# Optimization experiments

Hardware: AMD Instinct MI355X
Metric: run time of the kernel (lower is better)

Reference implementation:

```python
import jax, jax.numpy as jnp
import numpy as np

B, H, W, C = 4, 180, 320, 64
ATTN_SCALE = 0.125  # C ** -0.5
EPS = 1e-6  # flax LayerNorm default epsilon


def _layer_norm(x, scale, bias):
    mu = jnp.mean(x, axis=-1, keepdims=True)
    var = jnp.mean(jnp.square(x - mu), axis=-1, keepdims=True)
    return (x - mu) * jax.lax.rsqrt(var + EPS) * scale + bias


def setup_inputs() -> dict:
    key = jax.random.key(0)
    ks = jax.random.split(key, 8)
    w_init = 1.0 / np.sqrt(C)  # lecun_normal-ish scale for CxC dense kernels
    return {
        "x_l": jax.random.normal(ks[0], (B, H, W, C), jnp.float32),
        "x_r": jax.random.normal(ks[1], (B, H, W, C), jnp.float32),
        "ln_l_scale": jnp.ones((C,), jnp.float32),
        "ln_l_bias": jnp.zeros((C,), jnp.float32),
        "ln_r_scale": jnp.ones((C,), jnp.float32),
        "ln_r_bias": jnp.zeros((C,), jnp.float32),
        "w_ql": jax.random.normal(ks[2], (C, C), jnp.float32) * w_init,
        "b_ql": jnp.zeros((C,), jnp.float32),
        "w_qr": jax.random.normal(ks[3], (C, C), jnp.float32) * w_init,
        "b_qr": jnp.zeros((C,), jnp.float32),
        "w_vl": jax.random.normal(ks[4], (C, C), jnp.float32) * w_init,
        "b_vl": jnp.zeros((C,), jnp.float32),
        "w_vr": jax.random.normal(ks[5], (C, C), jnp.float32) * w_init,
        "b_vr": jnp.zeros((C,), jnp.float32),
        "beta": jax.random.normal(ks[6], (1, 1, 1, C), jnp.float32) * 0.1,
        "gamma": jax.random.normal(ks[7], (1, 1, 1, C), jnp.float32) * 0.1,
    }


def reference(x_l, x_r, ln_l_scale, ln_l_bias, ln_r_scale, ln_r_bias,
              w_ql, b_ql, w_qr, b_qr, w_vl, b_vl, w_vr, b_vr, beta, gamma):
    # Projections (attention runs along the width axis, per (b, h) scanline)
    q_l = _layer_norm(x_l, ln_l_scale, ln_l_bias) @ w_ql + b_ql   # [B,H,W,C]
    q_r = _layer_norm(x_r, ln_r_scale, ln_r_bias) @ w_qr + b_qr   # [B,H,W,C]
    v_l = x_l @ w_vl + b_vl                                       # [B,H,W,C]
    v_r = x_r @ w_vr + b_vr                                       # [B,H,W,C]

    # Shared score matrix: [B, H, W_l, W_r]
    attn = jnp.einsum('bhlc,bhrc->bhlr', q_l, q_r) * ATTN_SCALE

    # Row softmax (over W_r) attends right->left
    f_r2l = jnp.einsum('bhlr,bhrc->bhlc', jax.nn.softmax(attn, axis=-1), v_r) * beta
    # Column softmax (over W_l) attends left->right
    f_l2r = jnp.einsum('bhlr,bhlc->bhrc', jax.nn.softmax(attn, axis=-2), v_l) * gamma

    return (x_l + f_r2l, x_r + f_l2r)
```

## Files before the change

### kernel.cpp

```cpp
#include <hip/hip_runtime.h>
#include <hip/hip_bf16.h>

#define NB 4
#define NH 180
#define NW 320
#define NC 64
#define NSCAN (NB*NH)
#define NROWS (NB*NH*NW)
#define NELEM ((size_t)NROWS*NC)

using short8  = __attribute__((ext_vector_type(8))) short;
using floatx4 = __attribute__((ext_vector_type(4))) float;

__device__ __forceinline__ float bflo(unsigned int u) { return __uint_as_float(u << 16); }
__device__ __forceinline__ float bfhi(unsigned int u) { return __uint_as_float(u & 0xffff0000u); }

__device__ __forceinline__ unsigned short fbf(float f) {
    __hip_bfloat16 h = __float2bfloat16(f);
    unsigned short s; __builtin_memcpy(&s, &h, 2); return s;
}
__device__ __forceinline__ unsigned int packbf(float lo, float hi) {
    return (unsigned int)fbf(lo) | ((unsigned int)fbf(hi) << 16);
}

#define SCALE_LOG2E 0.18033688011112042f

__global__ __launch_bounds__(256) void proj_kernel(
    const float* __restrict__ xl, const float* __restrict__ xr,
    const float* __restrict__ lsl, const float* __restrict__ lbl,
    const float* __restrict__ lsr, const float* __restrict__ lbr,
    const float* __restrict__ wql, const float* __restrict__ bql,
    const float* __restrict__ wqr, const float* __restrict__ bqr,
    const float* __restrict__ wvl, const float* __restrict__ bvl,
    const float* __restrict__ wvr, const float* __restrict__ bvr,
    __hip_bfloat16* __restrict__ ql, __hip_bfloat16* __restrict__ qr,
    __hip_bfloat16* __restrict__ vlT, __hip_bfloat16* __restrict__ vrT)
{
    const int p    = blockIdx.y;
    const int t    = threadIdx.x;
    const int row0 = blockIdx.x * 256;

    const float* src  = (p == 0 || p == 2) ? xl : xr;
    const float* Wm   = (p == 0) ? wql : (p == 1) ? wqr : (p == 2) ? wvl : wvr;
    const float* bias = (p == 0) ? bql : (p == 1) ? bqr : (p == 2) ? bvl : bvr;
    __hip_bfloat16* dst = (p == 0) ? ql : (p == 1) ? qr : (p == 2) ? vlT : vrT;
    const bool doLN = (p < 2);
    const float* lns = (p == 0) ? lsl : lsr;
    const float* lnb = (p == 0) ? lbl : lbr;
    const float oscale = (p == 0) ? SCALE_LOG2E : 1.0f;

    __shared__ __align__(16) __hip_bfloat16 sA[256 * 72];
    __shared__ __align__(16) __hip_bfloat16 sWt[64 * 72];
    __shared__ float sLs[64], sLb[64], sBias[64];

    if (t < 64) {
        sLs[t]   = doLN ? lns[t] : 1.0f;
        sLb[t]   = doLN ? lnb[t] : 0.0f;
        sBias[t] = bias[t];
    }
    {
        const int k  = t >> 2;
        const int c0 = (t & 3) * 16;
        const float4* wrow = (const float4*)(Wm + k * NC + c0);
        float wv[16];
#pragma unroll
        for (int j = 0; j < 4; ++j) {
            float4 w4 = wrow[j];
            wv[4*j] = w4.x; wv[4*j+1] = w4.y; wv[4*j+2] = w4.z; wv[4*j+3] = w4.w;
        }
#pragma unroll
        for (int j = 0; j < 16; ++j)
            sWt[(c0 + j) * 72 + k] = __float2bfloat16(wv[j]);
    }
    __syncthreads();

    {
        const float4* x4 = (const float4*)(src + (size_t)(row0 + t) * NC);
        float f[64];
#pragma unroll
        for (int j = 0; j < 16; ++j) {
            float4 v = x4[j];
            f[4*j] = v.x; f[4*j+1] = v.y; f[4*j+2] = v.z; f[4*j+3] = v.w;
        }
        if (doLN) {
            float s = 0.f, s2 = 0.f;
#pragma unroll
            for (int c = 0; c < 64; ++c) { s += f[c]; s2 = fmaf(f[c], f[c], s2); }
            const float mu   = s * (1.0f / 64.0f);
            const float var  = s2 * (1.0f / 64.0f) - mu * mu;
            const float rstd = rsqrtf(var + 1e-6f);
#pragma unroll
            for (int c = 0; c < 64; ++c) f[c] = (f[c] - mu) * rstd * sLs[c] + sLb[c];
        }
        unsigned int* arow = (unsigned int*)&sA[t * 72];
#pragma unroll
        for (int j = 0; j < 32; ++j) arow[j] = packbf(f[2*j], f[2*j+1]);
    }
    __syncthreads();

    const int lane = t & 63;
    const int wv_  = t >> 6;
    const int quad = lane >> 4;
    const int mn   = lane & 15;

    short8 bfr[4][2];
#pragma unroll
    for (int nt = 0; nt < 4; ++nt)
#pragma unroll
        for (int ks = 0; ks < 2; ++ks)
            bfr[nt][ks] = *(const short8*)&sWt[(nt * 16 + mn) * 72 + ks * 32 + quad * 8];

#pragma unroll
    for (int mt = 0; mt < 4; ++mt) {
        const int rl = wv_ * 64 + mt * 16 + mn;
        short8 a0 = *(const short8*)&sA[rl * 72 +      quad * 8];
        short8 a1 = *(const short8*)&sA[rl * 72 + 32 + quad * 8];
#pragma unroll
        for (int nt = 0; nt < 4; ++nt) {
            floatx4 c = {0.f, 0.f, 0.f, 0.f};
            c = __builtin_amdgcn_mfma_f32_16x16x32_bf16(a0, bfr[nt][0], c, 0, 0, 0);
            c = __builtin_amdgcn_mfma_f32_16x16x32_bf16(a1, bfr[nt][1], c, 0, 0, 0);
            const int col = nt * 16 + mn;
            const float bb = sBias[col];
            if (p < 2) {
#pragma unroll
                for (int i = 0; i < 4; ++i) {
                    const int rowl = wv_ * 64 + mt * 16 + quad * 4 + i;
                    dst[(size_t)(row0 + rowl) * NC + col] =
                        __float2bfloat16((c[i] + bb) * oscale);
                }
            } else {
#pragma unroll
                for (int i = 0; i < 4; ++i) {
                    const unsigned grow = (unsigned)(row0 + wv_ * 64 + mt * 16 + quad * 4 + i);
                    const unsigned sc   = grow / 320u;
                    const unsigned wr   = grow - sc * 320u;
                    dst[(size_t)sc * (NC * NW) + (unsigned)col * NW + wr] =
                        __float2bfloat16(c[i] + bb);
                }
            }
        }
    }
}

__global__ __launch_bounds__(256) void attn_kernel(
    const __hip_bfloat16* __restrict__ ql, const __hip_bfloat16* __restrict__ qr,
    const __hip_bfloat16* __restrict__ vlT, const __hip_bfloat16* __restrict__ vrT,
    const float* __restrict__ xl, const float* __restrict__ xr,
    const float* __restrict__ beta, const float* __restrict__ gamma,
    float* __restrict__ out)
{
    const int flat = blockIdx.x + 5 * (blockIdx.y + 720 * blockIdx.z);
    const int g    = (flat & 7) * 900 + (flat >> 3);
    const int mt   = g % 5;
    const int s2   = g / 5;
    const int p    = s2 & 1;
    const int scan = s2 >> 1;

    const int t    = threadIdx.x;
    const int lane = t & 63;
    const int w    = t >> 6;
    const int quad = lane >> 4;
    const int mn   = lane & 15;
    const int m0   = mt * 64;

    const __hip_bfloat16* Q  = (p ? qr  : ql ) + (size_t)scan * (NW * NC);
    const __hip_bfloat16* K  = (p ? ql  : qr ) + (size_t)scan * (NW * NC);
    const __hip_bfloat16* VT = (p ? vlT : vrT) + (size_t)scan * (NC * NW);
    const float* xS = p ? xr : xl;
    const float* gv = p ? gamma : beta;

    __shared__ __align__(16) __hip_bfloat16 sQP[64 * 72];
    __shared__ __align__(16) char sU[18432];
    __shared__ float sRS[64];
    __hip_bfloat16* sK  = (__hip_bfloat16*)sU;
    __hip_bfloat16* sVt = (__hip_bfloat16*)(sU + 9216);
    float* sO = (float*)sU;

    const int sr  = t >> 2;
    const int sc0 = (t & 3) * 16;

    uint4 rk0, rk1, rv0, rv1;
    {
        const uint4* gk = (const uint4*)(K + (size_t)sr * NC + sc0);
        rk0 = gk[0]; rk1 = gk[1];
        const uint4* gt = (const uint4*)(VT + (size_t)sr * NW + sc0);
        rv0 = gt[0]; rv1 = gt[1];
    }

    {
        const uint4* gq = (const uint4*)(Q + (size_t)(m0 + sr) * NC + sc0);
        uint4 a = gq[0], b = gq[1];
        uint4* d = (uint4*)&sQP[sr * 72 + sc0];
        d[0] = a; d[1] = b;
    }
    __syncthreads();

    const short8 qa0 = *(const short8*)&sQP[(w * 16 + mn) * 72 +      quad * 8];
    const short8 qa1 = *(const short8*)&sQP[(w * 16 + mn) * 72 + 32 + quad * 8];

    floatx4 acc[4];
#pragma unroll
    for (int nt = 0; nt < 4; ++nt) acc[nt] = (floatx4){0.f, 0.f, 0.f, 0.f};
    float rs = 0.f;

    for (int rb = 0; rb < NW; rb += 64) {
        __syncthreads();
        {
            uint4* dk = (uint4*)&sK [sr * 72 + sc0]; dk[0] = rk0; dk[1] = rk1;
            uint4* dv = (uint4*)&sVt[sr * 72 + sc0]; dv[0] = rv0; dv[1] = rv1;
        }
        __syncthreads();

        if (rb + 64 < NW) {
            const uint4* gk = (const uint4*)(K + (size_t)(rb + 64 + sr) * NC + sc0);
            rk0 = gk[0]; rk1 = gk[1];
            const uint4* gt = (const uint4*)(VT + (size_t)sr * NW + (rb + 64) + sc0);
            rv0 = gt[0]; rv1 = gt[1];
        }

        __builtin_amdgcn_s_setprio(1);
#pragma unroll
        for (int rt = 0; rt < 4; ++rt) {
            short8 ka0 = *(const short8*)&sK[(rt * 16 + mn) * 72 +      quad * 8];
            short8 ka1 = *(const short8*)&sK[(rt * 16 + mn) * 72 + 32 + quad * 8];
            floatx4 s = {0.f, 0.f, 0.f, 0.f};
            s = __builtin_amdgcn_mfma_f32_16x16x32_bf16(ka0, qa0, s, 0, 0, 0);
            s = __builtin_amdgcn_mfma_f32_16x16x32_bf16(ka1, qa1, s, 0, 0, 0);
            const unsigned c0 = packbf(exp2f(s[0]), exp2f(s[1]));
            const unsigned c1 = packbf(exp2f(s[2]), exp2f(s[3]));
            rs += bflo(c0) + bfhi(c0) + bflo(c1) + bfhi(c1);
            uint2 pk; pk.x = c0; pk.y = c1;
            *(uint2*)&sQP[(w * 16 + mn) * 72 + rt * 16 + quad * 4] = pk;
        }

#pragma unroll
        for (int ks = 0; ks < 2; ++ks) {
            short8 pa = *(const short8*)&sQP[(w * 16 + mn) * 72 + ks * 32 + quad * 8];
#pragma unroll
            for (int nt = 0; nt < 4; ++nt) {
                short8 vb = *(const short8*)&sVt[(nt * 16 + mn) * 72 + ks * 32 + quad * 8];
                acc[nt] = __builtin_amdgcn_mfma_f32_16x16x32_bf16(pa, vb, acc[nt], 0, 0, 0);
            }
        }
        __builtin_amdgcn_s_setprio(0);
    }

    rs += __shfl_xor(rs, 16);
    rs += __shfl_xor(rs, 32);

    __syncthreads();

    if (lane < 16) sRS[w * 16 + lane] = 1.0f / rs;
#pragma unroll
    for (int nt = 0; nt < 4; ++nt)
#pragma unroll
        for (int i = 0; i < 4; ++i)
            sO[(w * 16 + quad * 4 + i) * 68 + nt * 16 + mn] = acc[nt][i];
    __syncthreads();

    {
        const int m = t >> 2, c0 = (t & 3) * 16;
        const float inv = sRS[m];
        const int grow = scan * NW + m0 + m;
        const float4* xg = (const float4*)(xS + (size_t)grow * NC + c0);
        const float4* gg = (const float4*)(gv + c0);
        const float4* so = (const float4*)&sO[m * 68 + c0];
        float4* og = (float4*)(out + (p ? NELEM : (size_t)0) + (size_t)grow * NC + c0);
#pragma unroll
        for (int j = 0; j < 4; ++j) {
            float4 xv = xg[j];
            float4 gvv = gg[j];
            float4 ov = so[j];
            float4 o;
            o.x = xv.x + ov.x * inv * gvv.x;
            o.y = xv.y + ov.y * inv * gvv.y;
            o.z = xv.z + ov.z * inv * gvv.z;
            o.w = xv.w + ov.w * inv * gvv.w;
            og[j] = o;
        }
    }
}

extern "C" void kernel_launch(void* const* d_in, const int* in_sizes, int n_in,
                              void* d_out, int out_size, void* d_ws, size_t ws_size,
                              hipStream_t stream)
{
    const float* xl  = (const float*)d_in[0];
    const float* xr  = (const float*)d_in[1];
    const float* lsl = (const float*)d_in[2];
    const float* lbl = (const float*)d_in[3];
    const float* lsr = (const float*)d_in[4];
    const float* lbr = (const float*)d_in[5];
    const float* wql = (const float*)d_in[6];
    const float* bql = (const float*)d_in[7];
    const float* wqr = (const float*)d_in[8];
    const float* bqr = (const float*)d_in[9];
    const float* wvl = (const float*)d_in[10];
    const float* bvl = (const float*)d_in[11];
    const float* wvr = (const float*)d_in[12];
    const float* bvr = (const float*)d_in[13];
    const float* beta  = (const float*)d_in[14];
    const float* gamma = (const float*)d_in[15];

    __hip_bfloat16* ws   = (__hip_bfloat16*)d_ws;
    __hip_bfloat16* ql_  = ws;
    __hip_bfloat16* qr_  = ws + NELEM;
    __hip_bfloat16* vlT_ = ws + 2 * NELEM;
    __hip_bfloat16* vrT_ = ws + 3 * NELEM;

    proj_kernel<<<dim3(NROWS / 256, 4, 1), 256, 0, stream>>>(
        xl, xr, lsl, lbl, lsr, lbr, wql, bql, wqr, bqr, wvl, bvl, wvr, bvr,
        ql_, qr_, vlT_, vrT_);

    attn_kernel<<<dim3(5, NSCAN, 2), 256, 0, stream>>>(
        ql_, qr_, vlT_, vrT_, xl, xr, beta, gamma, (float*)d_out);
}
```

Before: 375.0 us.

## Read K/V fragments directly from global, per-wave LDS buffers, swizzle proj grid

The attention kernel no longer stages K and V^T tiles through shared memory with block-wide barriers. Each wave now loads its MFMA operand fragments straight from global memory (relying on L1/L2 caching) and keeps a private LDS buffer for the P tile and output staging, which removes every __syncthreads. The softmax row sum is now accumulated in fp32 before bf16 rounding. Launch bounds are raised to 5 blocks per SM to favor occupancy. The projection kernel's block order is also remapped with an XCD-style interleave. The trade-off is that each wave issues redundant global loads instead of sharing one staged copy, which adds cache traffic.

```diff
diff --git a/kernel.cpp b/kernel.cpp
--- a/kernel.cpp
+++ b/kernel.cpp
@@ -36,9 +36,15 @@
     __hip_bfloat16* __restrict__ ql, __hip_bfloat16* __restrict__ qr,
     __hip_bfloat16* __restrict__ vlT, __hip_bfloat16* __restrict__ vrT)
 {
-    const int p    = blockIdx.y;
+    const int flat = blockIdx.x + 900 * blockIdx.y;
+    const int g    = (flat & 7) * 450 + (flat >> 3);
+    const int kind = g & 1;
+    const int pairid = g >> 1;
+    const int side = pairid & 1;
+    const int tile = pairid >> 1;
+    const int p    = side + 2 * kind;
     const int t    = threadIdx.x;
-    const int row0 = blockIdx.x * 256;
+    const int row0 = tile * 256;
 
     const float* src  = (p == 0 || p == 2) ? xl : xr;
     const float* Wm   = (p == 0) ? wql : (p == 1) ? wqr : (p == 2) ? wvl : wvr;
@@ -143,7 +149,7 @@
     }
 }
 
-__global__ __launch_bounds__(256) void attn_kernel(
+__global__ __launch_bounds__(256, 5) void attn_kernel(
     const __hip_bfloat16* __restrict__ ql, const __hip_bfloat16* __restrict__ qr,
     const __hip_bfloat16* __restrict__ vlT, const __hip_bfloat16* __restrict__ vrT,
     const float* __restrict__ xl, const float* __restrict__ xr,
@@ -170,34 +176,14 @@
     const float* xS = p ? xr : xl;
     const float* gv = p ? gamma : beta;
 
-    __shared__ __align__(16) __hip_bfloat16 sQP[64 * 72];
-    __shared__ __align__(16) char sU[18432];
+    __shared__ __align__(16) char sW[4 * 4608];
     __shared__ float sRS[64];
-    __hip_bfloat16* sK  = (__hip_bfloat16*)sU;
-    __hip_bfloat16* sVt = (__hip_bfloat16*)(sU + 9216);
-    float* sO = (float*)sU;
-
-    const int sr  = t >> 2;
-    const int sc0 = (t & 3) * 16;
-
-    uint4 rk0, rk1, rv0, rv1;
-    {
-        const uint4* gk = (const uint4*)(K + (size_t)sr * NC + sc0);
-        rk0 = gk[0]; rk1 = gk[1];
-        const uint4* gt = (const uint4*)(VT + (size_t)sr * NW + sc0);
-        rv0 = gt[0]; rv1 = gt[1];
-    }
-
-    {
-        const uint4* gq = (const uint4*)(Q + (size_t)(m0 + sr) * NC + sc0);
-        uint4 a = gq[0], b = gq[1];
-        uint4* d = (uint4*)&sQP[sr * 72 + sc0];
-        d[0] = a; d[1] = b;
-    }
-    __syncthreads();
-
-    const short8 qa0 = *(const short8*)&sQP[(w * 16 + mn) * 72 +      quad * 8];
-    const short8 qa1 = *(const short8*)&sQP[(w * 16 + mn) * 72 + 32 + quad * 8];
+    __hip_bfloat16* sP  = (__hip_bfloat16*)(sW + w * 4608);
+    float*          sOw = (float*)(sW + w * 4608);
+
+    const __hip_bfloat16* qrow = Q + (size_t)(m0 + w * 16 + mn) * NC;
+    const short8 qa0 = *(const short8*)(qrow + quad * 8);
+    const short8 qa1 = *(const short8*)(qrow + 32 + quad * 8);
 
     floatx4 acc[4];
 #pragma unroll
@@ -205,41 +191,30 @@
     float rs = 0.f;
 
     for (int rb = 0; rb < NW; rb += 64) {
-        __syncthreads();
-        {
-            uint4* dk = (uint4*)&sK [sr * 72 + sc0]; dk[0] = rk0; dk[1] = rk1;
-            uint4* dv = (uint4*)&sVt[sr * 72 + sc0]; dv[0] = rv0; dv[1] = rv1;
-        }
-        __syncthreads();
-
-        if (rb + 64 < NW) {
-            const uint4* gk = (const uint4*)(K + (size_t)(rb + 64 + sr) * NC + sc0);
-            rk0 = gk[0]; rk1 = gk[1];
-            const uint4* gt = (const uint4*)(VT + (size_t)sr * NW + (rb + 64) + sc0);
-            rv0 = gt[0]; rv1 = gt[1];
-        }
-
         __builtin_amdgcn_s_setprio(1);
 #pragma unroll
         for (int rt = 0; rt < 4; ++rt) {
-            short8 ka0 = *(const short8*)&sK[(rt * 16 + mn) * 72 +      quad * 8];
-            short8 ka1 = *(const short8*)&sK[(rt * 16 + mn) * 72 + 32 + quad * 8];
+            const __hip_bfloat16* kr = K + (size_t)(rb + rt * 16 + mn) * NC + quad * 8;
+            const short8 ka0 = *(const short8*)kr;
+            const short8 ka1 = *(const short8*)(kr + 32);
             floatx4 s = {0.f, 0.f, 0.f, 0.f};
             s = __builtin_amdgcn_mfma_f32_16x16x32_bf16(ka0, qa0, s, 0, 0, 0);
             s = __builtin_amdgcn_mfma_f32_16x16x32_bf16(ka1, qa1, s, 0, 0, 0);
-            const unsigned c0 = packbf(exp2f(s[0]), exp2f(s[1]));
-            const unsigned c1 = packbf(exp2f(s[2]), exp2f(s[3]));
-            rs += bflo(c0) + bfhi(c0) + bflo(c1) + bfhi(c1);
-            uint2 pk; pk.x = c0; pk.y = c1;
-            *(uint2*)&sQP[(w * 16 + mn) * 72 + rt * 16 + quad * 4] = pk;
+            const float e0 = exp2f(s[0]), e1 = exp2f(s[1]);
+            const float e2 = exp2f(s[2]), e3 = exp2f(s[3]);
+            rs += (e0 + e1) + (e2 + e3);
+            uint2 pk; pk.x = packbf(e0, e1); pk.y = packbf(e2, e3);
+            *(uint2*)&sP[mn * 72 + rt * 16 + quad * 4] = pk;
         }
 
 #pragma unroll
         for (int ks = 0; ks < 2; ++ks) {
-            short8 pa = *(const short8*)&sQP[(w * 16 + mn) * 72 + ks * 32 + quad * 8];
+            const short8 pa = *(const short8*)&sP[mn * 72 + ks * 32 + quad * 8];
 #pragma unroll
             for (int nt = 0; nt < 4; ++nt) {
-                short8 vb = *(const short8*)&sVt[(nt * 16 + mn) * 72 + ks * 32 + quad * 8];
+                const __hip_bfloat16* vr =
+                    VT + (size_t)(nt * 16 + mn) * NW + rb + ks * 32 + quad * 8;
+                const short8 vb = *(const short8*)vr;
                 acc[nt] = __builtin_amdgcn_mfma_f32_16x16x32_bf16(pa, vb, acc[nt], 0, 0, 0);
             }
         }
@@ -249,15 +224,13 @@
     rs += __shfl_xor(rs, 16);
     rs += __shfl_xor(rs, 32);
 
-    __syncthreads();
-
     if (lane < 16) sRS[w * 16 + lane] = 1.0f / rs;
+
 #pragma unroll
     for (int nt = 0; nt < 4; ++nt)
 #pragma unroll
         for (int i = 0; i < 4; ++i)
-            sO[(w * 16 + quad * 4 + i) * 68 + nt * 16 + mn] = acc[nt][i];
-    __syncthreads();
+            sOw[(quad * 4 + i) * 68 + nt * 16 + mn] = acc[nt][i];
 
     {
         const int m = t >> 2, c0 = (t & 3) * 16;
@@ -265,7 +238,8 @@
         const int grow = scan * NW + m0 + m;
         const float4* xg = (const float4*)(xS + (size_t)grow * NC + c0);
         const float4* gg = (const float4*)(gv + c0);
-        const float4* so = (const float4*)&sO[m * 68 + c0];
+        const float4* so = (const float4*)((const float*)(sW + (m >> 4) * 4608)
+                                           + (m & 15) * 68 + c0);
         float4* og = (float4*)(out + (p ? NELEM : (size_t)0) + (size_t)grow * NC + c0);
 #pragma unroll
         for (int j = 0; j < 4; ++j) {
@@ -309,7 +283,7 @@
     __hip_bfloat16* vlT_ = ws + 2 * NELEM;
     __hip_bfloat16* vrT_ = ws + 3 * NELEM;
 
-    proj_kernel<<<dim3(NROWS / 256, 4, 1), 256, 0, stream>>>(
+    proj_kernel<<<dim3(900, 4, 1), 256, 0, stream>>>(
         xl, xr, lsl, lbl, lsr, lbr, wql, bql, wqr, bqr, wvl, bvl, wvr, bvr,
         ql_, qr_, vlT_, vrT_);
 
```

New measurement: 555.9 us. +48.2%, slower.

## Keep softmax probabilities in registers via permlane swaps instead of LDS round-trip

Applied to the files above, without the earlier changes.

The attention kernel no longer writes exponentiated scores to shared memory and reads them back as the MFMA A operand. It rearranges the packed bf16 values across lanes with permlane32/permlane16 swaps, and loads Q fragments straight from global memory. This drops the sQP buffer, one barrier and the LDS traffic, and adds a launch-bounds occupancy hint. The projection grid is also remapped so blocks interleave tiles and sides across XCDs, and the row sum now accumulates fp32 values rather than bf16-rounded ones, which slightly changes numerics.

```diff
diff --git a/kernel.cpp b/kernel.cpp
--- a/kernel.cpp
+++ b/kernel.cpp
@@ -11,9 +11,7 @@
 
 using short8  = __attribute__((ext_vector_type(8))) short;
 using floatx4 = __attribute__((ext_vector_type(4))) float;
-
-__device__ __forceinline__ float bflo(unsigned int u) { return __uint_as_float(u << 16); }
-__device__ __forceinline__ float bfhi(unsigned int u) { return __uint_as_float(u & 0xffff0000u); }
+using uint2v  = __attribute__((ext_vector_type(2))) unsigned int;
 
 __device__ __forceinline__ unsigned short fbf(float f) {
     __hip_bfloat16 h = __float2bfloat16(f);
@@ -21,6 +19,29 @@
 }
 __device__ __forceinline__ unsigned int packbf(float lo, float hi) {
     return (unsigned int)fbf(lo) | ((unsigned int)fbf(hi) << 16);
+}
+
+__device__ __forceinline__ void swap32(unsigned& a, unsigned& b, int lane) {
+#if __has_builtin(__builtin_amdgcn_permlane32_swap)
+    uint2v r = __builtin_amdgcn_permlane32_swap(a, b, false, false);
+    a = r.x; b = r.y;
+#else
+    unsigned as = __shfl_xor(a, 32), bs = __shfl_xor(b, 32);
+    unsigned na = (lane < 32) ? a : bs;
+    unsigned nb = (lane < 32) ? as : b;
+    a = na; b = nb;
+#endif
+}
+__device__ __forceinline__ void swap16(unsigned& a, unsigned& b, int lane) {
+#if __has_builtin(__builtin_amdgcn_permlane16_swap)
+    uint2v r = __builtin_amdgcn_permlane16_swap(a, b, false, false);
+    a = r.x; b = r.y;
+#else
+    unsigned as = __shfl_xor(a, 16), bs = __shfl_xor(b, 16);
+    unsigned na = (lane & 16) ? bs : a;
+    unsigned nb = (lane & 16) ? b : as;
+    a = na; b = nb;
+#endif
 }
 
 #define SCALE_LOG2E 0.18033688011112042f
@@ -36,9 +57,15 @@
     __hip_bfloat16* __restrict__ ql, __hip_bfloat16* __restrict__ qr,
     __hip_bfloat16* __restrict__ vlT, __hip_bfloat16* __restrict__ vrT)
 {
-    const int p    = blockIdx.y;
+    const int flat = blockIdx.x + 900 * blockIdx.y;
+    const int g    = (flat & 7) * 450 + (flat >> 3);
+    const int kind = g & 1;
+    const int pairid = g >> 1;
+    const int side = pairid & 1;
+    const int tile = pairid >> 1;
+    const int p    = side + 2 * kind;
     const int t    = threadIdx.x;
-    const int row0 = blockIdx.x * 256;
+    const int row0 = tile * 256;
 
     const float* src  = (p == 0 || p == 2) ? xl : xr;
     const float* Wm   = (p == 0) ? wql : (p == 1) ? wqr : (p == 2) ? wvl : wvr;
@@ -143,7 +170,7 @@
     }
 }
 
-__global__ __launch_bounds__(256) void attn_kernel(
+__global__ __launch_bounds__(256, 6) void attn_kernel(
     const __hip_bfloat16* __restrict__ ql, const __hip_bfloat16* __restrict__ qr,
     const __hip_bfloat16* __restrict__ vlT, const __hip_bfloat16* __restrict__ vrT,
     const float* __restrict__ xl, const float* __restrict__ xr,
@@ -170,7 +197,6 @@
     const float* xS = p ? xr : xl;
     const float* gv = p ? gamma : beta;
 
-    __shared__ __align__(16) __hip_bfloat16 sQP[64 * 72];
     __shared__ __align__(16) char sU[18432];
     __shared__ float sRS[64];
     __hip_bfloat16* sK  = (__hip_bfloat16*)sU;
@@ -188,16 +214,9 @@
         rv0 = gt[0]; rv1 = gt[1];
     }
 
-    {
-        const uint4* gq = (const uint4*)(Q + (size_t)(m0 + sr) * NC + sc0);
-        uint4 a = gq[0], b = gq[1];
-        uint4* d = (uint4*)&sQP[sr * 72 + sc0];
-        d[0] = a; d[1] = b;
-    }
-    __syncthreads();
-
-    const short8 qa0 = *(const short8*)&sQP[(w * 16 + mn) * 72 +      quad * 8];
-    const short8 qa1 = *(const short8*)&sQP[(w * 16 + mn) * 72 + 32 + quad * 8];
+    const __hip_bfloat16* qrow = Q + (size_t)(m0 + w * 16 + mn) * NC;
+    const short8 qa0 = *(const short8*)(qrow + quad * 8);
+    const short8 qa1 = *(const short8*)(qrow + 32 + quad * 8);
 
     floatx4 acc[4];
 #pragma unroll
@@ -220,6 +239,7 @@
         }
 
         __builtin_amdgcn_s_setprio(1);
+        unsigned w0[4], w1[4];
 #pragma unroll
         for (int rt = 0; rt < 4; ++rt) {
             short8 ka0 = *(const short8*)&sK[(rt * 16 + mn) * 72 +      quad * 8];
@@ -227,16 +247,21 @@
             floatx4 s = {0.f, 0.f, 0.f, 0.f};
             s = __builtin_amdgcn_mfma_f32_16x16x32_bf16(ka0, qa0, s, 0, 0, 0);
             s = __builtin_amdgcn_mfma_f32_16x16x32_bf16(ka1, qa1, s, 0, 0, 0);
-            const unsigned c0 = packbf(exp2f(s[0]), exp2f(s[1]));
-            const unsigned c1 = packbf(exp2f(s[2]), exp2f(s[3]));
-            rs += bflo(c0) + bfhi(c0) + bflo(c1) + bfhi(c1);
-            uint2 pk; pk.x = c0; pk.y = c1;
-            *(uint2*)&sQP[(w * 16 + mn) * 72 + rt * 16 + quad * 4] = pk;
+            const float e0 = exp2f(s[0]), e1 = exp2f(s[1]);
+            const float e2 = exp2f(s[2]), e3 = exp2f(s[3]);
+            rs += (e0 + e1) + (e2 + e3);
+            w0[rt] = packbf(e0, e1);
+            w1[rt] = packbf(e2, e3);
         }
 
 #pragma unroll
         for (int ks = 0; ks < 2; ++ks) {
-            short8 pa = *(const short8*)&sQP[(w * 16 + mn) * 72 + ks * 32 + quad * 8];
+            unsigned a0 = w0[2 * ks], b0 = w0[2 * ks + 1];
+            swap32(a0, b0, lane); swap16(a0, b0, lane);
+            unsigned a1 = w1[2 * ks], b1 = w1[2 * ks + 1];
+            swap32(a1, b1, lane); swap16(a1, b1, lane);
+            uint4 pu; pu.x = a0; pu.y = a1; pu.z = b0; pu.w = b1;
+            short8 pa; __builtin_memcpy(&pa, &pu, 16);
 #pragma unroll
             for (int nt = 0; nt < 4; ++nt) {
                 short8 vb = *(const short8*)&sVt[(nt * 16 + mn) * 72 + ks * 32 + quad * 8];
@@ -257,7 +282,6 @@
 #pragma unroll
         for (int i = 0; i < 4; ++i)
             sO[(w * 16 + quad * 4 + i) * 68 + nt * 16 + mn] = acc[nt][i];
-    __syncthreads();
 
     {
         const int m = t >> 2, c0 = (t & 3) * 16;
@@ -309,7 +333,7 @@
     __hip_bfloat16* vlT_ = ws + 2 * NELEM;
     __hip_bfloat16* vrT_ = ws + 3 * NELEM;
 
-    proj_kernel<<<dim3(NROWS / 256, 4, 1), 256, 0, stream>>>(
+    proj_kernel<<<dim3(900, 4, 1), 256, 0, stream>>>(
         xl, xr, lsl, lbl, lsr, lbr, wql, bql, wqr, bqr, wvl, bvl, wvr, bvr,
         ql_, qr_, vlT_, vrT_);
 
```

New measurement: 364.0 us. -2.9%, faster.
